# Kernel optimization log

Hardware: AMD Instinct MI355X
Metric: run time of the kernel (lower is better)

## Reference

```python
import jax, jax.numpy as jnp
import numpy as np

HIDDEN = 4096
NUM_HEADS = 32
NUM_KV_HEADS = 8
HEAD_DIM = 128


def setup_inputs() -> dict:
    key = jax.random.key(0)
    k0, k1, k2, k3, k4 = jax.random.split(key, 5)
    B, S = 1, 2048
    s = 0.02
    return {
        "hidden_states": jax.random.normal(k0, (B, S, HIDDEN), dtype=jnp.float32),
        "Wq": jax.random.normal(k1, (HIDDEN, NUM_HEADS * HEAD_DIM), dtype=jnp.float32) * s,
        "Wk": jax.random.normal(k2, (HIDDEN, NUM_KV_HEADS * HEAD_DIM), dtype=jnp.float32) * s,
        "Wv": jax.random.normal(k3, (HIDDEN, NUM_KV_HEADS * HEAD_DIM), dtype=jnp.float32) * s,
        "Wo": jax.random.normal(k4, (NUM_HEADS * HEAD_DIM, HIDDEN), dtype=jnp.float32) * s,
    }


def reference(hidden_states, Wq, Wk, Wv, Wo):
    B, S, _ = hidden_states.shape
    n_rep = NUM_HEADS // NUM_KV_HEADS
    # Projections -> [B, H, S, D]
    q = (hidden_states @ Wq).reshape(B, S, NUM_HEADS, HEAD_DIM).transpose(0, 2, 1, 3)
    k = (hidden_states @ Wk).reshape(B, S, NUM_KV_HEADS, HEAD_DIM).transpose(0, 2, 1, 3)
    v = (hidden_states @ Wv).reshape(B, S, NUM_KV_HEADS, HEAD_DIM).transpose(0, 2, 1, 3)
    # GQA expansion: repeat_interleave KV heads to match query head count
    k = jnp.repeat(k, n_rep, axis=1)
    v = jnp.repeat(v, n_rep, axis=1)
    scale = HEAD_DIM ** -0.5
    # Full [B, H, S, S] attention scores (faithful to the naive reference)
    scores = jnp.einsum("bhqd,bhkd->bhqk", q, k) * scale
    causal = jnp.tril(jnp.ones((S, S), dtype=bool))
    scores = jnp.where(causal[None, None], scores, jnp.float32(-jnp.inf))
    probs = jax.nn.softmax(scores, axis=-1)
    out = jnp.einsum("bhqk,bhkd->bhqd", probs, v)
    out = out.transpose(0, 2, 1, 3).reshape(B, S, NUM_HEADS * HEAD_DIM)
    return out @ Wo
```

## Files before the change

### kernel.cpp

```cpp
#include <hip/hip_runtime.h>
#include <hip/hip_bf16.h>

typedef __bf16 bf16;
typedef __bf16 bf16x4 __attribute__((ext_vector_type(4)));
typedef __bf16 bf16x8 __attribute__((ext_vector_type(8)));
typedef float  f32x4  __attribute__((ext_vector_type(4)));

#define SEQ  2048
#define HID  4096
#define QKVN 6144

__device__ __forceinline__ void gload_lds16(const void* g, void* l) {
  __builtin_amdgcn_global_load_lds(
      (const __attribute__((address_space(1))) void*)g,
      (__attribute__((address_space(3))) void*)l, 16, 0, 0);
}

__global__ __launch_bounds__(256) void cast_f32_bf16(const float* __restrict__ in,
                                                     bf16* __restrict__ out, int n) {
  int i = (blockIdx.x * 256 + threadIdx.x) * 4;
  int stride = gridDim.x * 256 * 4;
  for (; i < n; i += stride) {
    float4 v = *(const float4*)(in + i);
    bf16x4 o;
    o[0] = (bf16)v.x; o[1] = (bf16)v.y; o[2] = (bf16)v.z; o[3] = (bf16)v.w;
    *(bf16x4*)(out + i) = o;
  }
}

__global__ __launch_bounds__(256) void transpose_cast(const float* __restrict__ W,
                                                      bf16* __restrict__ Wt,
                                                      int N, int roff) {
  __shared__ float tile[32][33];
  int k0 = blockIdx.y * 32;
  int n0 = blockIdx.x * 32;
  int t = threadIdx.x;
  int r = t >> 5, c = t & 31;
#pragma unroll
  for (int p = 0; p < 4; ++p)
    tile[r + p * 8][c] = W[(size_t)(k0 + r + p * 8) * N + n0 + c];
  __syncthreads();
#pragma unroll
  for (int p = 0; p < 4; ++p)
    Wt[(size_t)(roff + n0 + r + p * 8) * 4096 + k0 + c] = (bf16)tile[c][r + p * 8];
}

__global__ __launch_bounds__(256) void transpose_v(const bf16* __restrict__ QKV,
                                                   bf16* __restrict__ Vt_g) {
  __shared__ bf16 tile[32][33];
  int s0 = blockIdx.x * 32;
  int d0 = blockIdx.y * 32;
  int g  = blockIdx.z;
  int t = threadIdx.x;
  int r = t >> 5, c = t & 31;
#pragma unroll
  for (int p = 0; p < 4; ++p)
    tile[r + p * 8][c] = QKV[(size_t)(s0 + r + p * 8) * QKVN + 5120 + g * 128 + d0 + c];
  __syncthreads();
#pragma unroll
  for (int p = 0; p < 4; ++p)
    Vt_g[(size_t)(g * 128 + d0 + r + p * 8) * SEQ + s0 + c] = tile[c][r + p * 8];
}

template <typename OUT_T>
__global__ __launch_bounds__(256) void gemm_bt(const bf16* __restrict__ A,
                                               const bf16* __restrict__ Bt,
                                               OUT_T* __restrict__ C,
                                               int K, int ldc) {
  __shared__ __align__(16) bf16 Abuf[128 * 32];
  __shared__ __align__(16) bf16 Bbuf[128 * 32];
  int m0 = blockIdx.y * 128, n0 = blockIdx.x * 128;
  int tid = threadIdx.x, w = tid >> 6, lane = tid & 63;
  int wr = w >> 1, wc = w & 1;
  int l15 = lane & 15, l4 = lane >> 4;
  f32x4 acc[4][4] = {};
  const int nk = K >> 5;
  for (int kt = 0; kt < nk; ++kt) {
    int k0 = kt << 5;
#pragma unroll
    for (int p = 0; p < 2; ++p) {
      int elem = p * 2048 + w * 512 + lane * 8;
      int row = elem >> 5, col = elem & 31;
      gload_lds16(A + (size_t)(m0 + row) * K + k0 + col, (char*)Abuf + 2 * elem);
      gload_lds16(Bt + (size_t)(n0 + row) * K + k0 + col, (char*)Bbuf + 2 * elem);
    }
    __syncthreads();
    bf16x8 af[4], bfr[4];
#pragma unroll
    for (int m = 0; m < 4; ++m)
      af[m] = *(const bf16x8*)(Abuf + (wr * 64 + m * 16 + l15) * 32 + l4 * 8);
#pragma unroll
    for (int n = 0; n < 4; ++n)
      bfr[n] = *(const bf16x8*)(Bbuf + (wc * 64 + n * 16 + l15) * 32 + l4 * 8);
#pragma unroll
    for (int m = 0; m < 4; ++m)
#pragma unroll
      for (int n = 0; n < 4; ++n)
        acc[m][n] = __builtin_amdgcn_mfma_f32_16x16x32_bf16(af[m], bfr[n], acc[m][n], 0, 0, 0);
    __syncthreads();
  }
#pragma unroll
  for (int m = 0; m < 4; ++m)
#pragma unroll
    for (int n = 0; n < 4; ++n)
#pragma unroll
      for (int i = 0; i < 4; ++i) {
        int row = m0 + wr * 64 + m * 16 + l4 * 4 + i;
        int col = n0 + wc * 64 + n * 16 + l15;
        C[(size_t)row * ldc + col] = (OUT_T)acc[m][n][i];
      }
}

__global__ __launch_bounds__(256) void attn_kernel(const bf16* __restrict__ QKV,
                                                   const bf16* __restrict__ Vt_g,
                                                   bf16* __restrict__ attn) {
  __shared__ __align__(16) bf16 Klds[64 * 128];
  __shared__ __align__(16) bf16 Vlds[128 * 64];
  __shared__ __align__(16) bf16 Plds[4 * 16 * 64];
  const int bid = blockIdx.x;
  const int g = bid & 7;
  const int slot_ = bid >> 3;
  const int h = g * 4 + (slot_ & 3);
  const int qb = slot_ >> 2;
  const int q0 = qb * 64;
  const int tid = threadIdx.x, w = tid >> 6, lane = tid & 63;
  const int l15 = lane & 15, l4 = lane >> 4;
  const int wq0 = q0 + w * 16;
  const int qcol = h * 128;
  const int kcol = 4096 + g * 128;
  const float scale = 0.08838834764831845f;
  const float LOG2E = 1.4426950408889634f;

  bf16x8 aq[4];
#pragma unroll
  for (int kc = 0; kc < 4; ++kc)
    aq[kc] = *(const bf16x8*)(QKV + (size_t)(wq0 + l15) * QKVN + qcol + kc * 32 + l4 * 8);

  f32x4 acc_o[8] = {};
  float mrow[4], lrow[4];
#pragma unroll
  for (int i = 0; i < 4; ++i) { mrow[i] = -1e30f; lrow[i] = 0.f; }

  const bf16* Vhead = Vt_g + (size_t)g * 128 * SEQ;

  const int nkb = qb + 1;
  for (int kbi = 0; kbi < nkb; ++kbi) {
    int kb = kbi * 64;
#pragma unroll
    for (int p = 0; p < 4; ++p) {
      int ck = p * 256 + tid;
      int krow = ck >> 4, kslot = ck & 15;
      int ksl = kslot ^ (krow & 7);
      gload_lds16((const char*)(QKV + (size_t)(kb + krow) * QKVN + kcol) + ksl * 16,
                  (char*)Klds + ck * 16);
      int cv = p * 256 + tid;
      int vrow = cv >> 3, vslot = cv & 7;
      int vsl = vslot ^ (vrow & 7);
      gload_lds16(Vhead + (size_t)vrow * SEQ + kb + vsl * 8,
                  (char*)Vlds + cv * 16);
    }
    __syncthreads();
    f32x4 accs[4] = {};
#pragma unroll
    for (int n = 0; n < 4; ++n) {
      int row_ = n * 16 + l15;
      int sw = (row_ & 7) << 4;
#pragma unroll
      for (int kc = 0; kc < 4; ++kc) {
        bf16x8 bk = *(const bf16x8*)((const char*)Klds + row_ * 256 + ((kc * 64 + l4 * 16) ^ sw));
        accs[n] = __builtin_amdgcn_mfma_f32_16x16x32_bf16(aq[kc], bk, accs[n], 0, 0, 0);
      }
    }
    bool needmask = (kb + 64 > wq0);
    float s[4][4];
#pragma unroll
    for (int n = 0; n < 4; ++n)
#pragma unroll
      for (int i = 0; i < 4; ++i) {
        float v = accs[n][i] * scale;
        if (needmask) {
          int ks = kb + n * 16 + l15;
          int qr = wq0 + l4 * 4 + i;
          if (ks > qr) v = -1e30f;
        }
        s[n][i] = v;
      }
    float fac[4], ps[4][4];
#pragma unroll
    for (int i = 0; i < 4; ++i) {
      float t = fmaxf(fmaxf(s[0][i], s[1][i]), fmaxf(s[2][i], s[3][i]));
      t = fmaxf(t, __shfl_xor(t, 1));
      t = fmaxf(t, __shfl_xor(t, 2));
      t = fmaxf(t, __shfl_xor(t, 4));
      t = fmaxf(t, __shfl_xor(t, 8));
      float mnew = fmaxf(mrow[i], t);
      fac[i] = exp2f((mrow[i] - mnew) * LOG2E);
      float psum = 0.f;
#pragma unroll
      for (int n = 0; n < 4; ++n) {
        float p = exp2f((s[n][i] - mnew) * LOG2E);
        ps[n][i] = p; psum += p;
      }
      psum += __shfl_xor(psum, 1);
      psum += __shfl_xor(psum, 2);
      psum += __shfl_xor(psum, 4);
      psum += __shfl_xor(psum, 8);
      lrow[i] = lrow[i] * fac[i] + psum;
      mrow[i] = mnew;
    }
#pragma unroll
    for (int n2 = 0; n2 < 8; ++n2)
#pragma unroll
      for (int i = 0; i < 4; ++i)
        acc_o[n2][i] *= fac[i];
    char* Pw = (char*)Plds + w * 2048;
#pragma unroll
    for (int n = 0; n < 4; ++n)
#pragma unroll
      for (int i = 0; i < 4; ++i) {
        int r = l4 * 4 + i;
        int b = (r * 128 + (n * 16 + l15) * 2) ^ ((r & 7) << 4);
        *(bf16*)(Pw + b) = (bf16)ps[n][i];
      }
    __builtin_amdgcn_sched_barrier(0);
    asm volatile("" ::: "memory");
    bf16x8 pa[2];
#pragma unroll
    for (int kc = 0; kc < 2; ++kc)
      pa[kc] = *(const bf16x8*)(Pw + (l15 * 128 + ((kc * 64 + l4 * 16) ^ ((l15 & 7) << 4))));
#pragma unroll
    for (int n2 = 0; n2 < 8; ++n2) {
      int row_ = n2 * 16 + l15;
      int sw = (row_ & 7) << 4;
#pragma unroll
      for (int kc = 0; kc < 2; ++kc) {
        bf16x8 bv = *(const bf16x8*)((const char*)Vlds + row_ * 128 + ((kc * 64 + l4 * 16) ^ sw));
        acc_o[n2] = __builtin_amdgcn_mfma_f32_16x16x32_bf16(pa[kc], bv, acc_o[n2], 0, 0, 0);
      }
    }
    __syncthreads();
  }
#pragma unroll
  for (int n2 = 0; n2 < 8; ++n2)
#pragma unroll
    for (int i = 0; i < 4; ++i) {
      int row = wq0 + l4 * 4 + i;
      int col = h * 128 + n2 * 16 + l15;
      attn[(size_t)row * 4096 + col] = (bf16)(acc_o[n2][i] / lrow[i]);
    }
}

extern "C" void kernel_launch(void* const* d_in, const int* in_sizes, int n_in,
                              void* d_out, int out_size, void* d_ws, size_t ws_size,
                              hipStream_t stream) {
  const float* X  = (const float*)d_in[0];
  const float* Wq = (const float*)d_in[1];
  const float* Wk = (const float*)d_in[2];
  const float* Wv = (const float*)d_in[3];
  const float* Wo = (const float*)d_in[4];
  float* out = (float*)d_out;

  const size_t XB_OFF  = 0;
  const size_t WT_OFF  = 16777216;
  const size_t VT_OFF  = WT_OFF + 33554432;
  const size_t QKV_OFF = 16777216 + 50331648;
  if (ws_size < (size_t)92274688) return;

  char* ws = (char*)d_ws;
  bf16* Xb    = (bf16*)(ws + XB_OFF);
  bf16* Wt    = (bf16*)(ws + WT_OFF);
  bf16* Vt_g  = (bf16*)(ws + VT_OFF);
  bf16* QKV   = (bf16*)(ws + QKV_OFF);
  bf16* attnb = Xb;

  cast_f32_bf16<<<2048, 256, 0, stream>>>(X, Xb, SEQ * HID);
  transpose_cast<<<dim3(4096 / 32, 4096 / 32), 256, 0, stream>>>(Wq, Wt, 4096, 0);
  transpose_cast<<<dim3(1024 / 32, 4096 / 32), 256, 0, stream>>>(Wk, Wt, 1024, 4096);
  transpose_cast<<<dim3(1024 / 32, 4096 / 32), 256, 0, stream>>>(Wv, Wt, 1024, 5120);
  gemm_bt<bf16><<<dim3(QKVN / 128, SEQ / 128), 256, 0, stream>>>(Xb, Wt, QKV, HID, QKVN);
  transpose_cast<<<dim3(4096 / 32, 4096 / 32), 256, 0, stream>>>(Wo, Wt, 4096, 0);
  transpose_v<<<dim3(SEQ / 32, 4, 8), 256, 0, stream>>>(QKV, Vt_g);
  attn_kernel<<<1024, 256, 0, stream>>>(QKV, Vt_g, attnb);
  gemm_bt<float><<<dim3(4096 / 128, SEQ / 128), 256, 0, stream>>>(attnb, Wt, out, HID, 4096);
}
```

Measured before the change: 440.5 us.

## Replace 128x128 GEMM with double-buffered swizzled 256x256 tile GEMM

Replaces the simple single-buffered 128x128 GEMM with a 512-thread 256x256-tile kernel. It double-buffers K=64 slices in LDS with XOR swizzling, interleaves async global-to-LDS loads with MFMA phases, raises wave priority around MFMA, and remaps block IDs across XCDs. The goal is to hide memory latency and raise tensor-core utilisation in the QKV and output projections. In exchange it uses 128KB of LDS and hardcodes K=4096 and a row stride of 4096, and launches fewer blocks (192 and 128), which may underfill 256 CUs.

```diff
diff --git a/kernel.cpp b/kernel.cpp
--- a/kernel.cpp
+++ b/kernel.cpp
@@ -62,50 +62,112 @@
     Vt_g[(size_t)(g * 128 + d0 + r + p * 8) * SEQ + s0 + c] = tile[c][r + p * 8];
 }
 
+#define RD_A(dst, base, moff) \
+  _Pragma("unroll") for (int m_ = 0; m_ < 4; ++m_) \
+  _Pragma("unroll") for (int kk_ = 0; kk_ < 2; ++kk_) \
+    dst[m_][kk_] = *(const bf16x8*)((base) + (wr * 128 + (moff + m_) * 16 + l15) * 128 + \
+                                    (((kk_ * 64) + l4 * 16) ^ swz));
+#define RD_B(dst, base, noff) \
+  _Pragma("unroll") for (int n_ = 0; n_ < 2; ++n_) \
+  _Pragma("unroll") for (int kk_ = 0; kk_ < 2; ++kk_) \
+    dst[n_][kk_] = *(const bf16x8*)((base) + (wc * 64 + (noff + n_) * 16 + l15) * 128 + \
+                                    (((kk_ * 64) + l4 * 16) ^ swz));
+#define MM(af, bf_, moff, noff) \
+  _Pragma("unroll") for (int m_ = 0; m_ < 4; ++m_) \
+  _Pragma("unroll") for (int n_ = 0; n_ < 2; ++n_) \
+  _Pragma("unroll") for (int kk_ = 0; kk_ < 2; ++kk_) \
+    acc[moff + m_][noff + n_] = __builtin_amdgcn_mfma_f32_16x16x32_bf16( \
+        af[m_][kk_], bf_[n_][kk_], acc[moff + m_][noff + n_], 0, 0, 0);
+#define PH_SYNC_MFMA_BEGIN \
+  asm volatile("" ::: "memory"); __builtin_amdgcn_s_barrier(); \
+  asm volatile("s_waitcnt lgkmcnt(0)" ::: "memory"); \
+  __builtin_amdgcn_s_setprio(1);
+#define PH_END \
+  __builtin_amdgcn_s_setprio(0); \
+  asm volatile("" ::: "memory"); __builtin_amdgcn_s_barrier(); asm volatile("" ::: "memory");
+
 template <typename OUT_T>
-__global__ __launch_bounds__(256) void gemm_bt(const bf16* __restrict__ A,
-                                               const bf16* __restrict__ Bt,
-                                               OUT_T* __restrict__ C,
-                                               int K, int ldc) {
-  __shared__ __align__(16) bf16 Abuf[128 * 32];
-  __shared__ __align__(16) bf16 Bbuf[128 * 32];
-  int m0 = blockIdx.y * 128, n0 = blockIdx.x * 128;
-  int tid = threadIdx.x, w = tid >> 6, lane = tid & 63;
-  int wr = w >> 1, wc = w & 1;
-  int l15 = lane & 15, l4 = lane >> 4;
-  f32x4 acc[4][4] = {};
-  const int nk = K >> 5;
-  for (int kt = 0; kt < nk; ++kt) {
-    int k0 = kt << 5;
-#pragma unroll
-    for (int p = 0; p < 2; ++p) {
-      int elem = p * 2048 + w * 512 + lane * 8;
-      int row = elem >> 5, col = elem & 31;
-      gload_lds16(A + (size_t)(m0 + row) * K + k0 + col, (char*)Abuf + 2 * elem);
-      gload_lds16(Bt + (size_t)(n0 + row) * K + k0 + col, (char*)Bbuf + 2 * elem);
-    }
-    __syncthreads();
-    bf16x8 af[4], bfr[4];
-#pragma unroll
-    for (int m = 0; m < 4; ++m)
-      af[m] = *(const bf16x8*)(Abuf + (wr * 64 + m * 16 + l15) * 32 + l4 * 8);
+__global__ __launch_bounds__(512, 2) void gemm256(const bf16* __restrict__ A,
+                                                  const bf16* __restrict__ Bt,
+                                                  OUT_T* __restrict__ C,
+                                                  int NB, int ldc) {
+  __shared__ __align__(16) char lds[131072];
+  const int bid = blockIdx.x, nwg = gridDim.x;
+  const int cpx = nwg >> 3;
+  const int wid = (bid & 7) * cpx + (bid >> 3);
+  const int mb = wid / NB, nb = wid % NB;
+  const int m0 = mb << 8, n0 = nb << 8;
+  const int tid = threadIdx.x;
+  const int w = tid >> 6, lane = tid & 63;
+  const int wr = w >> 2, wc = w & 3;
+  const int l15 = lane & 15, l4 = lane >> 4;
+  const int swz = (l15 & 7) << 4;
+
+  char* const A0c = lds;
+  char* const B0c = lds + 32768;
+  char* const A1c = lds + 65536;
+  char* const B1c = lds + 98304;
+
+  auto stage = [&](const bf16* __restrict__ g, int grow0, int k0, char* dst) {
+#pragma unroll
+    for (int j = 0; j < 2; ++j) {
+      int c = tid + (j << 9);
+      int row = c >> 3, slot = c & 7;
+      gload_lds16((const char*)(g + ((size_t)(grow0 + row) << 12) + k0) +
+                      ((slot ^ (row & 7)) << 4),
+                  dst + c * 16);
+    }
+  };
+
+  f32x4 acc[8][4] = {};
+  bf16x8 a0[4][2], a1[4][2], b0[2][2], b1[2][2];
+
+  stage(A,  m0,        0,  A0c);
+  stage(A,  m0 + 128,  0,  A0c + 16384);
+  stage(Bt, n0,        0,  B0c);
+  stage(Bt, n0 + 128,  0,  B0c + 16384);
+  stage(A,  m0,        64, A1c);
+  stage(A,  m0 + 128,  64, A1c + 16384);
+  asm volatile("s_waitcnt vmcnt(4)" ::: "memory");
+  __builtin_amdgcn_s_barrier();
+
+  for (int it = 0; it < 32; ++it) {
+    const int k1 = (2 * it + 1) << 6;
+    const int k2 = (2 * it + 2) << 6;
+    const int k3 = (2 * it + 3) << 6;
+    const bool more = (it < 31);
+    RD_A(a0, A0c, 0); RD_B(b0, B0c, 0);
+    stage(Bt, n0, k1, B1c);
+    PH_SYNC_MFMA_BEGIN; MM(a0, b0, 0, 0); PH_END;
+    RD_A(a1, A0c, 4); RD_B(b1, B0c, 2);
+    stage(Bt, n0 + 128, k1, B1c + 16384);
+    PH_SYNC_MFMA_BEGIN; MM(a0, b1, 0, 2); PH_END;
+    if (more) stage(A, m0, k2, A0c);
+    PH_SYNC_MFMA_BEGIN; MM(a1, b0, 4, 0); PH_END;
+    if (more) stage(A, m0 + 128, k2, A0c + 16384);
+    if (it == 31) { asm volatile("s_waitcnt vmcnt(0)" ::: "memory"); }
+    else          { asm volatile("s_waitcnt vmcnt(4)" ::: "memory"); }
+    PH_SYNC_MFMA_BEGIN; MM(a1, b1, 4, 2); PH_END;
+    RD_A(a0, A1c, 0); RD_B(b0, B1c, 0);
+    if (more) stage(Bt, n0, k2, B0c);
+    PH_SYNC_MFMA_BEGIN; MM(a0, b0, 0, 0); PH_END;
+    RD_A(a1, A1c, 4); RD_B(b1, B1c, 2);
+    if (more) stage(Bt, n0 + 128, k2, B0c + 16384);
+    PH_SYNC_MFMA_BEGIN; MM(a0, b1, 0, 2); PH_END;
+    if (more) stage(A, m0, k3, A1c);
+    PH_SYNC_MFMA_BEGIN; MM(a1, b0, 4, 0); PH_END;
+    if (more) stage(A, m0 + 128, k3, A1c + 16384);
+    asm volatile("s_waitcnt vmcnt(4)" ::: "memory");
+    PH_SYNC_MFMA_BEGIN; MM(a1, b1, 4, 2); PH_END;
+  }
+
+#pragma unroll
+  for (int m = 0; m < 8; ++m)
 #pragma unroll
     for (int n = 0; n < 4; ++n)
-      bfr[n] = *(const bf16x8*)(Bbuf + (wc * 64 + n * 16 + l15) * 32 + l4 * 8);
-#pragma unroll
-    for (int m = 0; m < 4; ++m)
-#pragma unroll
-      for (int n = 0; n < 4; ++n)
-        acc[m][n] = __builtin_amdgcn_mfma_f32_16x16x32_bf16(af[m], bfr[n], acc[m][n], 0, 0, 0);
-    __syncthreads();
-  }
-#pragma unroll
-  for (int m = 0; m < 4; ++m)
-#pragma unroll
-    for (int n = 0; n < 4; ++n)
 #pragma unroll
       for (int i = 0; i < 4; ++i) {
-        int row = m0 + wr * 64 + m * 16 + l4 * 4 + i;
+        int row = m0 + wr * 128 + m * 16 + l4 * 4 + i;
         int col = n0 + wc * 64 + n * 16 + l15;
         C[(size_t)row * ldc + col] = (OUT_T)acc[m][n][i];
       }
@@ -277,9 +339,9 @@
   transpose_cast<<<dim3(4096 / 32, 4096 / 32), 256, 0, stream>>>(Wq, Wt, 4096, 0);
   transpose_cast<<<dim3(1024 / 32, 4096 / 32), 256, 0, stream>>>(Wk, Wt, 1024, 4096);
   transpose_cast<<<dim3(1024 / 32, 4096 / 32), 256, 0, stream>>>(Wv, Wt, 1024, 5120);
-  gemm_bt<bf16><<<dim3(QKVN / 128, SEQ / 128), 256, 0, stream>>>(Xb, Wt, QKV, HID, QKVN);
+  gemm256<bf16><<<192, 512, 0, stream>>>(Xb, Wt, QKV, 24, QKVN);
   transpose_cast<<<dim3(4096 / 32, 4096 / 32), 256, 0, stream>>>(Wo, Wt, 4096, 0);
   transpose_v<<<dim3(SEQ / 32, 4, 8), 256, 0, stream>>>(QKV, Vt_g);
   attn_kernel<<<1024, 256, 0, stream>>>(QKV, Vt_g, attnb);
-  gemm_bt<float><<<dim3(4096 / 128, SEQ / 128), 256, 0, stream>>>(attnb, Wt, out, HID, 4096);
-}
+  gemm256<float><<<128, 512, 0, stream>>>(attnb, Wt, out, 16, 4096);
+}
```

Result: slower. 524.9 us (+19.2%).

## Pair causal q-blocks per workgroup, share KV across two heads, double-buffer K/V

Applied to the files above, without the earlier changes.

The attention kernel now runs 512-thread workgroups that each handle two query heads of the same KV group and a balanced pair of query blocks (qb and 31-qb). Every workgroup therefore does an equal amount of causal work, and each staged K/V tile is reused by more waves. K/V tiles are double-buffered so the next tile's global-to-LDS load is issued before computing on the current one. The costs are twice the LDS per workgroup, more registers for two accumulator sets, and only 256 workgroups, which may underfill the CUs.

```diff
diff --git a/kernel.cpp b/kernel.cpp
--- a/kernel.cpp
+++ b/kernel.cpp
@@ -111,55 +111,61 @@
       }
 }
 
-__global__ __launch_bounds__(256) void attn_kernel(const bf16* __restrict__ QKV,
-                                                   const bf16* __restrict__ Vt_g,
-                                                   bf16* __restrict__ attn) {
-  __shared__ __align__(16) bf16 Klds[64 * 128];
-  __shared__ __align__(16) bf16 Vlds[128 * 64];
-  __shared__ __align__(16) bf16 Plds[4 * 16 * 64];
+__global__ __launch_bounds__(512, 2) void attn_kernel(const bf16* __restrict__ QKV,
+                                                      const bf16* __restrict__ Vt_g,
+                                                      bf16* __restrict__ attn) {
+  __shared__ __align__(16) bf16 Klds[2][64 * 128];
+  __shared__ __align__(16) bf16 Vlds[2][64 * 128];
+  __shared__ __align__(16) bf16 Plds[8 * 16 * 64];
   const int bid = blockIdx.x;
   const int g = bid & 7;
-  const int slot_ = bid >> 3;
-  const int h = g * 4 + (slot_ & 3);
-  const int qb = slot_ >> 2;
-  const int q0 = qb * 64;
+  const int rest = bid >> 3;
+  const int hg = rest & 1;
+  const int pair = rest >> 1;
+  const int qb_a = pair, qb_b = 31 - pair;
   const int tid = threadIdx.x, w = tid >> 6, lane = tid & 63;
+  const int hsel = w >> 2, qw = w & 3;
+  const int h = g * 4 + hg * 2 + hsel;
   const int l15 = lane & 15, l4 = lane >> 4;
-  const int wq0 = q0 + w * 16;
+  const int wqA = qb_a * 64 + qw * 16;
+  const int wqB = qb_b * 64 + qw * 16;
   const int qcol = h * 128;
   const int kcol = 4096 + g * 128;
   const float scale = 0.08838834764831845f;
   const float LOG2E = 1.4426950408889634f;
 
-  bf16x8 aq[4];
-#pragma unroll
-  for (int kc = 0; kc < 4; ++kc)
-    aq[kc] = *(const bf16x8*)(QKV + (size_t)(wq0 + l15) * QKVN + qcol + kc * 32 + l4 * 8);
-
-  f32x4 acc_o[8] = {};
-  float mrow[4], lrow[4];
-#pragma unroll
-  for (int i = 0; i < 4; ++i) { mrow[i] = -1e30f; lrow[i] = 0.f; }
-
   const bf16* Vhead = Vt_g + (size_t)g * 128 * SEQ;
 
-  const int nkb = qb + 1;
-  for (int kbi = 0; kbi < nkb; ++kbi) {
-    int kb = kbi * 64;
-#pragma unroll
-    for (int p = 0; p < 4; ++p) {
-      int ck = p * 256 + tid;
-      int krow = ck >> 4, kslot = ck & 15;
-      int ksl = kslot ^ (krow & 7);
-      gload_lds16((const char*)(QKV + (size_t)(kb + krow) * QKVN + kcol) + ksl * 16,
-                  (char*)Klds + ck * 16);
-      int cv = p * 256 + tid;
-      int vrow = cv >> 3, vslot = cv & 7;
-      int vsl = vslot ^ (vrow & 7);
-      gload_lds16(Vhead + (size_t)vrow * SEQ + kb + vsl * 8,
-                  (char*)Vlds + cv * 16);
-    }
-    __syncthreads();
+  bf16x8 aqA[4], aqB[4];
+#pragma unroll
+  for (int kc = 0; kc < 4; ++kc) {
+    aqA[kc] = *(const bf16x8*)(QKV + (size_t)(wqA + l15) * QKVN + qcol + kc * 32 + l4 * 8);
+    aqB[kc] = *(const bf16x8*)(QKV + (size_t)(wqB + l15) * QKVN + qcol + kc * 32 + l4 * 8);
+  }
+
+  f32x4 acc_oA[8] = {}, acc_oB[8] = {};
+  float mA[4], lA[4], mB[4], lB[4];
+#pragma unroll
+  for (int i = 0; i < 4; ++i) { mA[i] = -1e30f; lA[i] = 0.f; mB[i] = -1e30f; lB[i] = 0.f; }
+
+  auto stageKV = [&](int kb, int buf) {
+#pragma unroll
+    for (int j = 0; j < 2; ++j) {
+      int c = tid + (j << 9);
+      int krow = c >> 4, kslot = c & 15;
+      gload_lds16((const char*)(QKV + (size_t)(kb + krow) * QKVN + kcol) +
+                      ((kslot ^ (krow & 7)) << 4),
+                  (char*)Klds[buf] + c * 16);
+      int vrow = c >> 3, vslot = c & 7;
+      gload_lds16(Vhead + (size_t)vrow * SEQ + kb + ((vslot ^ (vrow & 7)) << 3),
+                  (char*)Vlds[buf] + c * 16);
+    }
+  };
+
+  auto compute_block = [&](const bf16x8* aq, f32x4* acc_o, float* mrow, float* lrow,
+                           int wq0, int kb, int cur) {
+    const char* Kbuf = (const char*)Klds[cur];
+    const char* Vbuf = (const char*)Vlds[cur];
     f32x4 accs[4] = {};
 #pragma unroll
     for (int n = 0; n < 4; ++n) {
@@ -167,7 +173,7 @@
       int sw = (row_ & 7) << 4;
 #pragma unroll
       for (int kc = 0; kc < 4; ++kc) {
-        bf16x8 bk = *(const bf16x8*)((const char*)Klds + row_ * 256 + ((kc * 64 + l4 * 16) ^ sw));
+        bf16x8 bk = *(const bf16x8*)(Kbuf + row_ * 256 + ((kc * 64 + l4 * 16) ^ sw));
         accs[n] = __builtin_amdgcn_mfma_f32_16x16x32_bf16(aq[kc], bk, accs[n], 0, 0, 0);
       }
     }
@@ -234,19 +240,33 @@
       int sw = (row_ & 7) << 4;
 #pragma unroll
       for (int kc = 0; kc < 2; ++kc) {
-        bf16x8 bv = *(const bf16x8*)((const char*)Vlds + row_ * 128 + ((kc * 64 + l4 * 16) ^ sw));
+        bf16x8 bv = *(const bf16x8*)(Vbuf + row_ * 128 + ((kc * 64 + l4 * 16) ^ sw));
         acc_o[n2] = __builtin_amdgcn_mfma_f32_16x16x32_bf16(pa[kc], bv, acc_o[n2], 0, 0, 0);
       }
     }
+    asm volatile("" ::: "memory");
+  };
+
+  stageKV(0, 0);
+  __syncthreads();
+
+  int cur = 0;
+  for (int kbi = 0; kbi <= qb_b; ++kbi) {
+    int kb = kbi * 64;
+    if (kbi < qb_b) stageKV(kb + 64, cur ^ 1);
+    if (kbi <= qb_a) compute_block(aqA, acc_oA, mA, lA, wqA, kb, cur);
+    compute_block(aqB, acc_oB, mB, lB, wqB, kb, cur);
     __syncthreads();
+    cur ^= 1;
   }
+
 #pragma unroll
   for (int n2 = 0; n2 < 8; ++n2)
 #pragma unroll
     for (int i = 0; i < 4; ++i) {
-      int row = wq0 + l4 * 4 + i;
-      int col = h * 128 + n2 * 16 + l15;
-      attn[(size_t)row * 4096 + col] = (bf16)(acc_o[n2][i] / lrow[i]);
+      int col = qcol + n2 * 16 + l15;
+      attn[(size_t)(wqA + l4 * 4 + i) * 4096 + col] = (bf16)(acc_oA[n2][i] / lA[i]);
+      attn[(size_t)(wqB + l4 * 4 + i) * 4096 + col] = (bf16)(acc_oB[n2][i] / lB[i]);
     }
 }
 
@@ -280,6 +300,6 @@
   gemm_bt<bf16><<<dim3(QKVN / 128, SEQ / 128), 256, 0, stream>>>(Xb, Wt, QKV, HID, QKVN);
   transpose_cast<<<dim3(4096 / 32, 4096 / 32), 256, 0, stream>>>(Wo, Wt, 4096, 0);
   transpose_v<<<dim3(SEQ / 32, 4, 8), 256, 0, stream>>>(QKV, Vt_g);
-  attn_kernel<<<1024, 256, 0, stream>>>(QKV, Vt_g, attnb);
+  attn_kernel<<<256, 512, 0, stream>>>(QKV, Vt_g, attnb);
   gemm_bt<float><<<dim3(4096 / 128, SEQ / 128), 256, 0, stream>>>(attnb, Wt, out, HID, 4096);
 }
```

Result: faster. 413.9 us (-6.0%).
